# Performance work log

Hardware: AMD Instinct MI355X
Metric: run time of the kernel (lower is better)

The kernel has to match this reference:

```python
import jax, jax.numpy as jnp
import numpy as np

PATCH_LEN = 16
PATCH_STRIDE = 8
DIM = 512
NUM_HEADS = 8
HEAD_DIM = DIM // NUM_HEADS
NUM_LAYERS = 4
MLP_HIDDEN = 4 * DIM
ROPE_BASE = 10000.0
LN_EPS = 1e-5


def setup_inputs() -> dict:
    key = jax.random.key(0)
    ks = jax.random.split(key, 20)
    B, T, C = 4, 8192, 7
    s = 0.02
    inp = {
        "x": jax.random.normal(ks[0], (B, T, C), dtype=jnp.float32),
        "W_emb": jax.random.normal(ks[1], (PATCH_LEN * C, DIM), dtype=jnp.float32) * s,
        "b_emb": jnp.zeros((DIM,), jnp.float32),
        "ln1_g": jnp.ones((NUM_LAYERS, DIM), jnp.float32),
        "ln1_b": jnp.zeros((NUM_LAYERS, DIM), jnp.float32),
        "W_qkv": jax.random.normal(ks[2], (NUM_LAYERS, DIM, 3 * DIM), dtype=jnp.float32) * s,
        "b_qkv": jnp.zeros((NUM_LAYERS, 3 * DIM), jnp.float32),
        "W_proj": jax.random.normal(ks[3], (NUM_LAYERS, DIM, DIM), dtype=jnp.float32) * s,
        "b_proj": jnp.zeros((NUM_LAYERS, DIM), jnp.float32),
        "ln2_g": jnp.ones((NUM_LAYERS, DIM), jnp.float32),
        "ln2_b": jnp.zeros((NUM_LAYERS, DIM), jnp.float32),
        "W_mlp1": jax.random.normal(ks[4], (NUM_LAYERS, DIM, MLP_HIDDEN), dtype=jnp.float32) * s,
        "b_mlp1": jnp.zeros((NUM_LAYERS, MLP_HIDDEN), jnp.float32),
        "W_mlp2": jax.random.normal(ks[5], (NUM_LAYERS, MLP_HIDDEN, DIM), dtype=jnp.float32) * s,
        "b_mlp2": jnp.zeros((NUM_LAYERS, DIM), jnp.float32),
        "lnf_g": jnp.ones((DIM,), jnp.float32),
        "lnf_b": jnp.zeros((DIM,), jnp.float32),
    }
    return inp


def _layer_norm(x, g, b):
    mu = jnp.mean(x, axis=-1, keepdims=True)
    var = jnp.mean(jnp.square(x - mu), axis=-1, keepdims=True)
    return (x - mu) * jax.lax.rsqrt(var + LN_EPS) * g + b


def _rotate_half(x):
    x1, x2 = jnp.split(x, 2, axis=-1)
    return jnp.concatenate((-x2, x1), axis=-1)


def _rope_cos_sin(seq_len):
    t = jnp.arange(seq_len, dtype=jnp.float32)
    inv_freq = 1.0 / (ROPE_BASE ** (jnp.arange(0, HEAD_DIM, 2, dtype=jnp.float32) / HEAD_DIM))
    freqs = jnp.outer(t, inv_freq)                      # [L, hd/2]
    emb = jnp.concatenate((freqs, freqs), axis=-1)      # [L, hd]
    return jnp.cos(emb), jnp.sin(emb)


def _forward(x, W_emb, b_emb, ln1_g, ln1_b, W_qkv, b_qkv, W_proj, b_proj,
             ln2_g, ln2_b, W_mlp1, b_mlp1, W_mlp2, b_mlp2, lnf_g, lnf_b):
    B, T, C = x.shape
    n = (T - PATCH_LEN) // PATCH_STRIDE + 1
    # torch unfold: [B, n, C, patch_len], then flattened as (C, patch_len)
    idx = jnp.arange(n)[:, None] * PATCH_STRIDE + jnp.arange(PATCH_LEN)[None, :]  # [n, P]
    patches = x[:, idx, :]                              # [B, n, P, C]
    patches = patches.transpose(0, 1, 3, 2).reshape(B, n, C * PATCH_LEN)
    emb = patches @ W_emb + b_emb                       # [B, n, D]

    cos, sin = _rope_cos_sin(n)                         # [n, hd]
    cos = cos[None, None, :, :]
    sin = sin[None, None, :, :]
    scale = HEAD_DIM ** -0.5

    h = emb
    for i in range(NUM_LAYERS):
        # --- attention ---
        y = _layer_norm(h, ln1_g[i], ln1_b[i])
        qkv = (y @ W_qkv[i] + b_qkv[i]).reshape(B, n, 3, NUM_HEADS, HEAD_DIM)
        qkv = qkv.transpose(2, 0, 3, 1, 4)              # [3, B, H, n, hd]
        q, k, v = qkv[0], qkv[1], qkv[2]
        q = q * cos + _rotate_half(q) * sin
        k = k * cos + _rotate_half(k) * sin
        attn = jax.nn.softmax(jnp.einsum('bhqd,bhkd->bhqk', q, k) * scale, axis=-1)
        o = jnp.einsum('bhqk,bhkd->bhqd', attn, v)      # [B, H, n, hd]
        o = o.transpose(0, 2, 1, 3).reshape(B, n, DIM)
        h = h + (o @ W_proj[i] + b_proj[i])
        # --- mlp ---
        y = _layer_norm(h, ln2_g[i], ln2_b[i])
        y = jax.nn.gelu(y @ W_mlp1[i] + b_mlp1[i], approximate=False)
        h = h + (y @ W_mlp2[i] + b_mlp2[i])

    x_out = _layer_norm(h, lnf_g, lnf_b)
    return emb, x_out


def reference(x, W_emb, b_emb, ln1_g, ln1_b, W_qkv, b_qkv, W_proj, b_proj,
              ln2_g, ln2_b, W_mlp1, b_mlp1, W_mlp2, b_mlp2, lnf_g, lnf_b):
    return _forward(x, W_emb, b_emb, ln1_g, ln1_b, W_qkv, b_qkv, W_proj, b_proj,
                    ln2_g, ln2_b, W_mlp1, b_mlp1, W_mlp2, b_mlp2, lnf_g, lnf_b)
```

## Files before the change

kernel.cpp:

```cpp
#include <hip/hip_runtime.h>
#include <hip/hip_bf16.h>
#include <math.h>

#define B_SZ 4
#define T_LEN 8192
#define C_IN 7
#define NPATCH 1023
#define DIM 512
#define NH 8
#define HD 64
#define NLAYERS 4
#define MLP_HID 2048
#define M_ROWS (B_SZ * NPATCH)
#define KEMB 128
#define LN_EPS 1e-5f

typedef __attribute__((ext_vector_type(8))) short short8;
typedef __attribute__((ext_vector_type(4))) float float4v;

static __device__ __forceinline__ unsigned short f2bf(float f) {
  __hip_bfloat16 h = __float2bfloat16(f);
  return *reinterpret_cast<unsigned short*>(&h);
}
static __device__ __forceinline__ float bf2f(unsigned short u) {
  return __uint_as_float(((unsigned)u) << 16);
}

__global__ __launch_bounds__(256) void patch_kernel(
    const float* __restrict__ x, unsigned short* __restrict__ Pm) {
  int idx = blockIdx.x * 256 + threadIdx.x;
  if (idx >= M_ROWS * KEMB) return;
  int row = idx >> 7, c = idx & 127;
  float v = 0.f;
  if (c < 112) {
    int b = row / NPATCH, i = row - b * NPATCH;
    int ci = c >> 4, p = c & 15;
    v = x[((size_t)b * T_LEN + (size_t)i * 8 + p) * C_IN + ci];
  }
  Pm[idx] = f2bf(v);
}

__global__ __launch_bounds__(256) void wemb_cvt_kernel(
    const float* __restrict__ W, unsigned short* __restrict__ Wt) {
  int idx = blockIdx.x * 256 + threadIdx.x;
  if (idx >= DIM * KEMB) return;
  int n = idx >> 7, k = idx & 127;
  float v = (k < 112) ? W[(size_t)k * DIM + n] : 0.f;
  Wt[idx] = f2bf(v);
}

template <bool BF>
__global__ __launch_bounds__(256) void ln_kernel(
    const float* __restrict__ in, const float* __restrict__ g,
    const float* __restrict__ bb, void* __restrict__ outv, int M) {
  int row = blockIdx.x * 4 + (threadIdx.x >> 6);
  if (row >= M) return;
  int lane = threadIdx.x & 63;
  const float* xr = in + (size_t)row * DIM;
  float v[8];
  float s = 0.f;
  #pragma unroll
  for (int k = 0; k < 8; ++k) { v[k] = xr[lane + 64 * k]; s += v[k]; }
  #pragma unroll
  for (int off = 32; off; off >>= 1) s += __shfl_down(s, off);
  s = __shfl(s, 0);
  float mu = s * (1.f / DIM);
  float q = 0.f;
  #pragma unroll
  for (int k = 0; k < 8; ++k) { float d = v[k] - mu; q = fmaf(d, d, q); }
  #pragma unroll
  for (int off = 32; off; off >>= 1) q += __shfl_down(q, off);
  q = __shfl(q, 0);
  float rstd = rsqrtf(q * (1.f / DIM) + LN_EPS);
  #pragma unroll
  for (int k = 0; k < 8; ++k) {
    int d = lane + 64 * k;
    float r = (v[k] - mu) * rstd * g[d] + bb[d];
    if (BF)
      ((unsigned short*)outv)[(size_t)row * DIM + d] = f2bf(r);
    else
      ((float*)outv)[(size_t)row * DIM + d] = r;
  }
}

__global__ __launch_bounds__(256) void wcvt_kernel(
    const float* __restrict__ W, unsigned short* __restrict__ Wt, int K, int N) {
  __shared__ float tile[32][33];
  int n0 = blockIdx.x * 32, k0 = blockIdx.y * 32, L = blockIdx.z;
  const float* Ws = W + (size_t)L * K * N;
  unsigned short* Wd = Wt + (size_t)L * K * N;
  int tx = threadIdx.x & 31, ty = threadIdx.x >> 5;
  #pragma unroll
  for (int i = 0; i < 4; ++i)
    tile[ty + i * 8][tx] = Ws[(size_t)(k0 + ty + i * 8) * N + n0 + tx];
  __syncthreads();
  #pragma unroll
  for (int i = 0; i < 4; ++i)
    Wd[(size_t)(n0 + ty + i * 8) * K + k0 + tx] = f2bf(tile[tx][ty + i * 8]);
}

__global__ __launch_bounds__(256) void rope_tab_kernel(float2* __restrict__ tab) {
  int idx = blockIdx.x * 256 + threadIdx.x;
  if (idx >= NPATCH * 32) return;
  int i = idx >> 5, j = idx & 31;
  float inv = powf(10000.0f, -(float)j * (1.0f / 32.0f));
  float sn, cs;
  sincosf((float)i * inv, &sn, &cs);
  tab[idx] = make_float2(cs, sn);
}

template <int TM, int TN, int EPI>
__global__ __launch_bounds__(256) void mfma_gemm(
    const unsigned short* __restrict__ A, const unsigned short* __restrict__ Bt,
    const float* __restrict__ bias, const float* __restrict__ res,
    float* __restrict__ Cf, float* __restrict__ Cf2,
    unsigned short* __restrict__ Cb, const float2* __restrict__ rtab,
    int M, int N, int K) {
  constexpr int WM = TM / 2, WN = TN / 2;
  constexpr int NI = WM / 16, NJ = WN / 16;
  constexpr int ACH = TM * 4;
  constexpr int TCH = (TM + TN) * 4;
  constexpr int CH = TCH / 256;
  __shared__ __align__(16) unsigned short As[2][TM][40];
  __shared__ __align__(16) unsigned short Bs[2][TN][40];
  const int bm = blockIdx.y * TM;
  const int bn = blockIdx.x * TN;
  const int tid = threadIdx.x;
  const int lane = tid & 63, wave = tid >> 6;
  const int quad = lane >> 4, l16 = lane & 15;
  const int wm = (wave & 1) * WM;
  const int wn = (wave >> 1) * WN;

  float4v acc[NI][NJ];
  #pragma unroll
  for (int i = 0; i < NI; ++i)
    #pragma unroll
    for (int j = 0; j < NJ; ++j)
      acc[i][j] = (float4v){0.f, 0.f, 0.f, 0.f};

  uint4 pr[CH];
  auto load_regs = [&](int kk) {
    #pragma unroll
    for (int it = 0; it < CH; ++it) {
      int c = tid + it * 256;
      if (c < ACH) {
        int row = c >> 2, ch = (c & 3) * 8;
        int gm = bm + row;
        pr[it] = make_uint4(0u, 0u, 0u, 0u);
        if (gm < M) pr[it] = *(const uint4*)(A + (size_t)gm * K + kk + ch);
      } else {
        int c2 = c - ACH;
        int row = c2 >> 2, ch = (c2 & 3) * 8;
        pr[it] = *(const uint4*)(Bt + (size_t)(bn + row) * K + kk + ch);
      }
    }
  };

  load_regs(0);
  int buf = 0;
  for (int k0 = 0; k0 < K; k0 += 32, buf ^= 1) {
    #pragma unroll
    for (int it = 0; it < CH; ++it) {
      int c = tid + it * 256;
      if (c < ACH)
        *(uint4*)&As[buf][c >> 2][(c & 3) * 8] = pr[it];
      else {
        int c2 = c - ACH;
        *(uint4*)&Bs[buf][c2 >> 2][(c2 & 3) * 8] = pr[it];
      }
    }
    if (k0 + 32 < K) load_regs(k0 + 32);
    __syncthreads();
    short8 af[NI], bfr[NJ];
    #pragma unroll
    for (int i = 0; i < NI; ++i)
      af[i] = *(const short8*)&As[buf][wm + i * 16 + l16][quad * 8];
    #pragma unroll
    for (int j = 0; j < NJ; ++j)
      bfr[j] = *(const short8*)&Bs[buf][wn + j * 16 + l16][quad * 8];
    __builtin_amdgcn_s_setprio(1);
    #pragma unroll
    for (int i = 0; i < NI; ++i)
      #pragma unroll
      for (int j = 0; j < NJ; ++j)
        acc[i][j] = __builtin_amdgcn_mfma_f32_16x16x32_bf16(
            af[i], bfr[j], acc[i][j], 0, 0, 0);
    __builtin_amdgcn_s_setprio(0);
  }

  if (EPI == 6) {
    const int sec = (bn + wn) >> 9;
    #pragma unroll
    for (int i = 0; i < NI; ++i) {
      int gm0 = bm + wm + i * 16 + quad * 4;
      #pragma unroll
      for (int r = 0; r < 4; ++r) {
        int gm = gm0 + r;
        if (gm >= M) continue;
        size_t rowoff = (size_t)gm * N;
        if (sec < 2) {
          int ip = gm; if (ip >= 2046) ip -= 2046; if (ip >= 1023) ip -= 1023;
          float sc = (sec == 0) ? 0.125f : 1.f;
          #pragma unroll
          for (int j = 0; j < NJ / 2; ++j) {
            int gn = bn + wn + j * 16 + l16;
            float v0 = acc[i][j][r] + bias[gn];
            float v1 = acc[i][j + NJ / 2][r] + bias[gn + 32];
            float2 t = rtab[ip * 32 + j * 16 + l16];
            Cb[rowoff + gn]      = f2bf((v0 * t.x - v1 * t.y) * sc);
            Cb[rowoff + gn + 32] = f2bf((v1 * t.x + v0 * t.y) * sc);
          }
        } else {
          #pragma unroll
          for (int j = 0; j < NJ; ++j) {
            int gn = bn + wn + j * 16 + l16;
            Cb[rowoff + gn] = f2bf(acc[i][j][r] + bias[gn]);
          }
        }
      }
    }
    return;
  }

  #pragma unroll
  for (int j = 0; j < NJ; ++j) {
    int gn = bn + wn + j * 16 + l16;
    float bv = bias[gn];
    #pragma unroll
    for (int i = 0; i < NI; ++i) {
      int gm0 = bm + wm + i * 16 + quad * 4;
      #pragma unroll
      for (int r = 0; r < 4; ++r) {
        int gm = gm0 + r;
        if (gm < M) {
          float v = acc[i][j][r] + bv;
          size_t off = (size_t)gm * N + gn;
          if (EPI == 1) {
            Cf[off] = v + res[off];
          } else if (EPI == 2) {
            Cb[off] = f2bf(0.5f * v * (1.f + erff(v * 0.70710678118f)));
          } else if (EPI == 3) {
            Cb[off] = f2bf(v);
          } else {
            Cf[off] = v;
            Cf2[off] = v;
          }
        }
      }
    }
  }
}

#define APITCH 72

__global__ __launch_bounds__(512, 4) void attn_kernel(
    const unsigned short* __restrict__ qkvb, unsigned short* __restrict__ o) {
  const int bid = blockIdx.x;
  const int xcd = bid & 7, slot = bid >> 3;
  const int qt0 = (slot & 15) * 64;
  const int gh = xcd + 8 * (slot >> 4);
  const int h = gh & 7, b = gh >> 3;

  const int tid = threadIdx.x;
  const int lane = tid & 63, wave = tid >> 6;
  const int quad = lane >> 4, l16 = lane & 15;
  const int half = wave >> 2, wq = wave & 3;

  __shared__ __align__(16) unsigned short Ks[2][64][APITCH];
  __shared__ __align__(16) unsigned short Vt[2][64][APITCH];
  __shared__ __align__(16) unsigned short Ps[8][16][APITCH];

  short8 aq0 = {0, 0, 0, 0, 0, 0, 0, 0}, aq1 = aq0;
  {
    int qrow = qt0 + wq * 16 + l16;
    if (qrow < NPATCH) {
      const uint4* qr = (const uint4*)(qkvb + (size_t)(b * NPATCH + qrow) * (3 * DIM) + h * HD + quad * 8);
      aq0 = __builtin_bit_cast(short8, qr[0]);
      aq1 = __builtin_bit_cast(short8, qr[4]);
    }
  }

  const int krow = tid >> 2, kc0 = (tid & 3) * 16;
  const int kp2 = tid & 63, dg = tid >> 6;
  uint4 pk0, pk1, pv0, pv1;
  auto load_kv = [&](int js) {
    pk0 = pk1 = pv0 = pv1 = make_uint4(0u, 0u, 0u, 0u);
    int jk = js + krow;
    if (jk < NPATCH) {
      const unsigned short* kb = qkvb + (size_t)(b * NPATCH + jk) * (3 * DIM) + DIM + h * HD;
      pk0 = *(const uint4*)(kb + kc0);
      pk1 = *(const uint4*)(kb + kc0 + 8);
    }
    int jv = js + 2 * kp2;
    const unsigned short* vb = qkvb + (size_t)(b * NPATCH + jv) * (3 * DIM) + 2 * DIM + h * HD + dg * 8;
    if (jv < NPATCH)     pv0 = *(const uint4*)vb;
    if (jv + 1 < NPATCH) pv1 = *(const uint4*)(vb + 3 * DIM);
  };

  load_kv(0);

  float4v accO[4];
  #pragma unroll
  for (int j2 = 0; j2 < 4; ++j2) accO[j2] = (float4v){0.f, 0.f, 0.f, 0.f};
  float m_run[4] = {-1e30f, -1e30f, -1e30f, -1e30f};
  float lp[4] = {0.f, 0.f, 0.f, 0.f};

  constexpr int NIT = (NPATCH + 127) / 128;
  for (int it = 0; it < NIT; ++it) {
    if (it > 0) __syncthreads();
    {
      *(uint4*)&Ks[krow >> 6][krow & 63][kc0] = pk0;
      *(uint4*)&Ks[krow >> 6][krow & 63][kc0 + 8] = pk1;
      unsigned short va[8], vb8[8];
      *(uint4*)&va[0] = pv0;
      *(uint4*)&vb8[0] = pv1;
      const int vh = kp2 >> 5, lp2 = kp2 & 31;
      #pragma unroll
      for (int u = 0; u < 8; ++u) {
        unsigned pk = (unsigned)va[u] | ((unsigned)vb8[u] << 16);
        *(unsigned*)&Vt[vh][dg * 8 + u][2 * lp2] = pk;
      }
    }
    __syncthreads();
    if (it + 1 < NIT) load_kv((it + 1) * 128);

    const int j0 = it * 128 + half * 64;

    float4v s[4];
    __builtin_amdgcn_s_setprio(1);
    #pragma unroll
    for (int j = 0; j < 4; ++j) {
      s[j] = (float4v){0.f, 0.f, 0.f, 0.f};
      short8 bk0 = *(const short8*)&Ks[half][j * 16 + l16][quad * 8];
      short8 bk1 = *(const short8*)&Ks[half][j * 16 + l16][32 + quad * 8];
      s[j] = __builtin_amdgcn_mfma_f32_16x16x32_bf16(aq0, bk0, s[j], 0, 0, 0);
      s[j] = __builtin_amdgcn_mfma_f32_16x16x32_bf16(aq1, bk1, s[j], 0, 0, 0);
    }
    __builtin_amdgcn_s_setprio(0);

    float mx[4];
    #pragma unroll
    for (int r = 0; r < 4; ++r)
      mx[r] = fmaxf(fmaxf(s[0][r], s[1][r]), fmaxf(s[2][r], s[3][r]));
    #pragma unroll
    for (int mask = 1; mask < 16; mask <<= 1)
      #pragma unroll
      for (int r = 0; r < 4; ++r)
        mx[r] = fmaxf(mx[r], __shfl_xor(mx[r], mask));
    float gmax = fmaxf(fmaxf(mx[0] - m_run[0], mx[1] - m_run[1]),
                       fmaxf(mx[2] - m_run[2], mx[3] - m_run[3]));
    if (!__all(gmax <= 8.f)) {
      #pragma unroll
      for (int r = 0; r < 4; ++r) {
        float mnew = fmaxf(m_run[r], mx[r]);
        float al = __expf(m_run[r] - mnew);
        m_run[r] = mnew;
        lp[r] *= al;
        #pragma unroll
        for (int j2 = 0; j2 < 4; ++j2) accO[j2][r] *= al;
      }
    }
    #pragma unroll
    for (int j = 0; j < 4; ++j) {
      bool valid = (j0 + j * 16 + l16) < NPATCH;
      #pragma unroll
      for (int r = 0; r < 4; ++r) {
        float p = valid ? __expf(s[j][r] - m_run[r]) : 0.f;
        lp[r] += p;
        Ps[wave][quad * 4 + r][j * 16 + l16] = f2bf(p);
      }
    }

    short8 pa0 = *(const short8*)&Ps[wave][l16][quad * 8];
    short8 pa1 = *(const short8*)&Ps[wave][l16][32 + quad * 8];
    __builtin_amdgcn_s_setprio(1);
    #pragma unroll
    for (int j2 = 0; j2 < 4; ++j2) {
      short8 v0 = *(const short8*)&Vt[half][j2 * 16 + l16][quad * 8];
      short8 v1 = *(const short8*)&Vt[half][j2 * 16 + l16][32 + quad * 8];
      accO[j2] = __builtin_amdgcn_mfma_f32_16x16x32_bf16(pa0, v0, accO[j2], 0, 0, 0);
      accO[j2] = __builtin_amdgcn_mfma_f32_16x16x32_bf16(pa1, v1, accO[j2], 0, 0, 0);
    }
    __builtin_amdgcn_s_setprio(0);
  }

  #pragma unroll
  for (int mask = 1; mask < 16; mask <<= 1)
    #pragma unroll
    for (int r = 0; r < 4; ++r)
      lp[r] += __shfl_xor(lp[r], mask);

  float* Pf = (float*)&Ps[0][0][0];
  __syncthreads();
  if (half == 1) {
    #pragma unroll
    for (int j2 = 0; j2 < 4; ++j2)
      #pragma unroll
      for (int r = 0; r < 4; ++r)
        Pf[((wq * 64 + lane) << 4) + j2 * 4 + r] = accO[j2][r];
    if (l16 == 0) {
      #pragma unroll
      for (int r = 0; r < 4; ++r) {
        Pf[4096 + ((wq * 16 + quad * 4 + r) << 1)]     = m_run[r];
        Pf[4096 + ((wq * 16 + quad * 4 + r) << 1) + 1] = lp[r];
      }
    }
  }
  __syncthreads();
  if (half == 0) {
    #pragma unroll
    for (int r = 0; r < 4; ++r) {
      float m1 = Pf[4096 + ((wq * 16 + quad * 4 + r) << 1)];
      float l1 = Pf[4096 + ((wq * 16 + quad * 4 + r) << 1) + 1];
      float M = fmaxf(m_run[r], m1);
      float w0 = __expf(m_run[r] - M), w1 = __expf(m1 - M);
      float inv = 1.f / (w0 * lp[r] + w1 * l1);
      int qi = qt0 + wq * 16 + quad * 4 + r;
      if (qi < NPATCH) {
        size_t off = (size_t)(b * NPATCH + qi) * DIM + h * HD + l16;
        #pragma unroll
        for (int j2 = 0; j2 < 4; ++j2) {
          float a1 = Pf[((wq * 64 + lane) << 4) + j2 * 4 + r];
          o[off + j2 * 16] = f2bf((w0 * accO[j2][r] + w1 * a1) * inv);
        }
      }
    }
  }
}

extern "C" void kernel_launch(void* const* d_in, const int* in_sizes, int n_in,
                              void* d_out, int out_size, void* d_ws, size_t ws_size,
                              hipStream_t stream) {
  const float* x      = (const float*)d_in[0];
  const float* W_emb  = (const float*)d_in[1];
  const float* b_emb  = (const float*)d_in[2];
  const float* ln1_g  = (const float*)d_in[3];
  const float* ln1_b  = (const float*)d_in[4];
  const float* W_qkv  = (const float*)d_in[5];
  const float* b_qkv  = (const float*)d_in[6];
  const float* W_proj = (const float*)d_in[7];
  const float* b_proj = (const float*)d_in[8];
  const float* ln2_g  = (const float*)d_in[9];
  const float* ln2_b  = (const float*)d_in[10];
  const float* W_mlp1 = (const float*)d_in[11];
  const float* b_mlp1 = (const float*)d_in[12];
  const float* W_mlp2 = (const float*)d_in[13];
  const float* b_mlp2 = (const float*)d_in[14];
  const float* lnf_g  = (const float*)d_in[15];
  const float* lnf_b  = (const float*)d_in[16];
  float* out = (float*)d_out;

  float* h              = (float*)d_ws;
  unsigned short* qkvb  = (unsigned short*)(h + (size_t)M_ROWS * DIM);
  unsigned short* midbf = qkvb;
  unsigned short* ybf   = qkvb + (size_t)M_ROWS * MLP_HID;
  unsigned short* obf   = ybf;
  unsigned short* wqkv_t  = ybf + (size_t)M_ROWS * DIM;
  unsigned short* wproj_t = wqkv_t  + (size_t)NLAYERS * DIM * 3 * DIM;
  unsigned short* wmlp1_t = wproj_t + (size_t)NLAYERS * DIM * DIM;
  unsigned short* wmlp2_t = wmlp1_t + (size_t)NLAYERS * DIM * MLP_HID;
  float2* rtab = (float2*)(wmlp2_t + (size_t)NLAYERS * MLP_HID * DIM);
  unsigned short* Pm    = (unsigned short*)(rtab + (size_t)NPATCH * 32);
  unsigned short* Wembt = Pm + (size_t)M_ROWS * KEMB;

  wcvt_kernel<<<dim3(3 * DIM / 32, DIM / 32, NLAYERS), 256, 0, stream>>>(W_qkv,  wqkv_t,  DIM, 3 * DIM);
  wcvt_kernel<<<dim3(DIM / 32, DIM / 32, NLAYERS),     256, 0, stream>>>(W_proj, wproj_t, DIM, DIM);
  wcvt_kernel<<<dim3(MLP_HID / 32, DIM / 32, NLAYERS), 256, 0, stream>>>(W_mlp1, wmlp1_t, DIM, MLP_HID);
  wcvt_kernel<<<dim3(DIM / 32, MLP_HID / 32, NLAYERS), 256, 0, stream>>>(W_mlp2, wmlp2_t, MLP_HID, DIM);
  rope_tab_kernel<<<(NPATCH * 32 + 255) / 256, 256, 0, stream>>>(rtab);
  patch_kernel<<<(M_ROWS * KEMB + 255) / 256, 256, 0, stream>>>(x, Pm);
  wemb_cvt_kernel<<<(DIM * KEMB + 255) / 256, 256, 0, stream>>>(W_emb, Wembt);

  const int MT64 = (M_ROWS + 63) / 64;
  const int MT128 = (M_ROWS + 127) / 128;
  const int LNG = (M_ROWS + 3) / 4;

  mfma_gemm<64, 64, 5><<<dim3(DIM / 64, MT64), 256, 0, stream>>>(
      Pm, Wembt, b_emb, nullptr, out, h, nullptr, nullptr, M_ROWS, DIM, KEMB);

  for (int L = 0; L < NLAYERS; ++L) {
    ln_kernel<true><<<LNG, 256, 0, stream>>>(h, ln1_g + L * DIM, ln1_b + L * DIM, ybf, M_ROWS);
    mfma_gemm<128, 128, 6><<<dim3(3 * DIM / 128, MT128), 256, 0, stream>>>(
        ybf, wqkv_t + (size_t)L * DIM * 3 * DIM, b_qkv + L * 3 * DIM,
        nullptr, nullptr, nullptr, qkvb, rtab, M_ROWS, 3 * DIM, DIM);
    attn_kernel<<<dim3(512), 512, 0, stream>>>(qkvb, obf);
    mfma_gemm<64, 64, 1><<<dim3(DIM / 64, MT64), 256, 0, stream>>>(
        obf, wproj_t + (size_t)L * DIM * DIM, b_proj + L * DIM,
        h, h, nullptr, nullptr, nullptr, M_ROWS, DIM, DIM);
    ln_kernel<true><<<LNG, 256, 0, stream>>>(h, ln2_g + L * DIM, ln2_b + L * DIM, ybf, M_ROWS);
    mfma_gemm<128, 128, 2><<<dim3(MLP_HID / 128, MT128), 256, 0, stream>>>(
        ybf, wmlp1_t + (size_t)L * DIM * MLP_HID, b_mlp1 + L * MLP_HID,
        nullptr, nullptr, nullptr, midbf, nullptr, M_ROWS, MLP_HID, DIM);
    mfma_gemm<64, 64, 1><<<dim3(DIM / 64, MT64), 256, 0, stream>>>(
        midbf, wmlp2_t + (size_t)L * MLP_HID * DIM, b_mlp2 + L * DIM,
        h, h, nullptr, nullptr, nullptr, M_ROWS, DIM, MLP_HID);
  }

  ln_kernel<false><<<LNG, 256, 0, stream>>>(h, lnf_g, lnf_b, out + (size_t)M_ROWS * DIM, M_ROWS);
}
```

Measured before the change: 683.9 us.

## Stage GEMM tiles with direct global-to-LDS loads and XOR-swizzled layout

The MFMA GEMM now loads A and B tiles with global_load_lds, which writes straight into shared memory instead of staging through registers and then storing to LDS. To replace the old padded rows, the LDS tiles are unpadded and use an XOR swizzle on the 16-byte column slot, and the fragment reads use the matching swizzled slot. The next tile is issued right after the barrier, so it overlaps with the MFMA work on the current buffer. This cuts VGPR use and LDS store instructions. It also drops the row bounds check on A, so edge tiles can read past M.

```diff
diff --git a/kernel.cpp b/kernel.cpp
--- a/kernel.cpp
+++ b/kernel.cpp
@@ -26,6 +26,12 @@
   return __uint_as_float(((unsigned)u) << 16);
 }
 
+static __device__ __forceinline__ void gload_lds16(const void* g, void* l) {
+  __builtin_amdgcn_global_load_lds(
+      (const __attribute__((address_space(1))) unsigned int*)g,
+      (__attribute__((address_space(3))) unsigned int*)l, 16, 0, 0);
+}
+
 __global__ __launch_bounds__(256) void patch_kernel(
     const float* __restrict__ x, unsigned short* __restrict__ Pm) {
   int idx = blockIdx.x * 256 + threadIdx.x;
@@ -118,11 +124,10 @@
     int M, int N, int K) {
   constexpr int WM = TM / 2, WN = TN / 2;
   constexpr int NI = WM / 16, NJ = WN / 16;
-  constexpr int ACH = TM * 4;
-  constexpr int TCH = (TM + TN) * 4;
-  constexpr int CH = TCH / 256;
-  __shared__ __align__(16) unsigned short As[2][TM][40];
-  __shared__ __align__(16) unsigned short Bs[2][TN][40];
+  constexpr int NCH = (TM + TN) / 16;
+  constexpr int CPW = NCH / 4;
+  __shared__ __align__(16) unsigned short As[2][TM][32];
+  __shared__ __align__(16) unsigned short Bs[2][TN][32];
   const int bm = blockIdx.y * TM;
   const int bn = blockIdx.x * TN;
   const int tid = threadIdx.x;
@@ -130,6 +135,8 @@
   const int quad = lane >> 4, l16 = lane & 15;
   const int wm = (wave & 1) * WM;
   const int wn = (wave >> 1) * WN;
+  const int lrow4 = lane >> 2, lc = lane & 3;
+  const int rslot = quad ^ ((l16 >> 1) & 3);
 
   float4v acc[NI][NJ];
   #pragma unroll
@@ -138,46 +145,37 @@
     for (int j = 0; j < NJ; ++j)
       acc[i][j] = (float4v){0.f, 0.f, 0.f, 0.f};
 
-  uint4 pr[CH];
-  auto load_regs = [&](int kk) {
-    #pragma unroll
-    for (int it = 0; it < CH; ++it) {
-      int c = tid + it * 256;
-      if (c < ACH) {
-        int row = c >> 2, ch = (c & 3) * 8;
-        int gm = bm + row;
-        pr[it] = make_uint4(0u, 0u, 0u, 0u);
-        if (gm < M) pr[it] = *(const uint4*)(A + (size_t)gm * K + kk + ch);
+  auto stage = [&](int bufI, int kk) {
+    #pragma unroll
+    for (int it = 0; it < CPW; ++it) {
+      int c = wave * CPW + it;
+      if (c < TM / 16) {
+        int row = c * 16 + lrow4;
+        int col16 = lc ^ ((row >> 1) & 3);
+        gload_lds16(A + (size_t)(bm + row) * K + kk + col16 * 8,
+                    &As[bufI][c * 16][0]);
       } else {
-        int c2 = c - ACH;
-        int row = c2 >> 2, ch = (c2 & 3) * 8;
-        pr[it] = *(const uint4*)(Bt + (size_t)(bn + row) * K + kk + ch);
+        int c2 = c - TM / 16;
+        int row = c2 * 16 + lrow4;
+        int col16 = lc ^ ((row >> 1) & 3);
+        gload_lds16(Bt + (size_t)(bn + row) * K + kk + col16 * 8,
+                    &Bs[bufI][c2 * 16][0]);
       }
     }
   };
 
-  load_regs(0);
+  stage(0, 0);
   int buf = 0;
   for (int k0 = 0; k0 < K; k0 += 32, buf ^= 1) {
-    #pragma unroll
-    for (int it = 0; it < CH; ++it) {
-      int c = tid + it * 256;
-      if (c < ACH)
-        *(uint4*)&As[buf][c >> 2][(c & 3) * 8] = pr[it];
-      else {
-        int c2 = c - ACH;
-        *(uint4*)&Bs[buf][c2 >> 2][(c2 & 3) * 8] = pr[it];
-      }
-    }
-    if (k0 + 32 < K) load_regs(k0 + 32);
     __syncthreads();
+    if (k0 + 32 < K) stage(buf ^ 1, k0 + 32);
     short8 af[NI], bfr[NJ];
     #pragma unroll
     for (int i = 0; i < NI; ++i)
-      af[i] = *(const short8*)&As[buf][wm + i * 16 + l16][quad * 8];
+      af[i] = *(const short8*)&As[buf][wm + i * 16 + l16][rslot * 8];
     #pragma unroll
     for (int j = 0; j < NJ; ++j)
-      bfr[j] = *(const short8*)&Bs[buf][wn + j * 16 + l16][quad * 8];
+      bfr[j] = *(const short8*)&Bs[buf][wn + j * 16 + l16][rslot * 8];
     __builtin_amdgcn_s_setprio(1);
     #pragma unroll
     for (int i = 0; i < NI; ++i)
```

New measurement: 644.2 us. 1.06x faster.
